# Performance work log

Measured on AMD Instinct MI355X. Metric: run time of the kernel, lower is better.

## Reference

```python
import jax, jax.numpy as jnp
import numpy as np

L, Q, B, F = 4096, 16, 4096, 2048


def setup_inputs() -> dict:
    key = jax.random.key(0)
    k1, k2, k3, k4, k5 = jax.random.split(key, 5)
    return {
        "input_features": jax.random.normal(k1, (B, F), dtype=jnp.float32),
        "queues": jax.random.normal(k2, (L, Q, F), dtype=jnp.float32),
        "labels": jax.random.randint(k3, (B,), 0, L, dtype=jnp.int32),
        "current_flags": jax.random.randint(k4, (L,), 0, Q, dtype=jnp.int32),
        "sample_idx": jax.random.randint(k5, (L,), 0, Q, dtype=jnp.int32),
    }


def reference(input_features, queues, labels, current_flags, sample_idx):
    # Faithful to Queues.update(): the momentum blend + normalize on each slot is
    # overwritten by the final `queue[label][flag] = input_feature`, so the net
    # effect is: for each sample i (in order), write input_features[i] into
    # queue[labels[i]] at slot (flags[labels[i]] + rank_i) % Q, where rank_i is
    b, f = input_features.shape
    l, q, _ = queues.shape
    idx = jnp.arange(b, dtype=jnp.int32)

    # rank of each sample within its label group (stable sort trick, no [B,L] one-hot)
    order = jnp.argsort(labels)                                   # stable in jax
    labels_sorted = labels[order]
    start = jax.ops.segment_min(idx, labels_sorted, num_segments=l)
    rank_sorted = idx - start[labels_sorted]
    rank = jnp.zeros((b,), jnp.int32).at[order].set(rank_sorted)

    pos = (current_flags[labels] + rank) % q                      # circular slot per sample

    flat_key = labels * q + pos
    winner = jax.ops.segment_max(idx, flat_key, num_segments=l * q)
    is_winner = winner[flat_key] == idx
    lab_w = jnp.where(is_winner, labels, l)                       # out-of-range -> dropped

    new_queues = queues.at[lab_w, pos].set(input_features, mode="drop")

    # advance circular pointers by per-label counts (state update, as in update())
    counts = jax.ops.segment_sum(jnp.ones((b,), jnp.int32), labels, num_segments=l)
    new_flags = (current_flags + counts) % q  # noqa: F841 (state; not sampled below)

    # get_features(): one random slot per label queue
    out = new_queues[jnp.arange(l), sample_idx]                   # [L, F]
    return out
```

## Files before the change

kernel.cpp:

```cpp
#include <hip/hip_runtime.h>

#define L_ 4096
#define Q_ 16
#define B_ 4096
#define F_ 2048
#define NC 16
#define CS 256


__global__ void k_rank(const int* __restrict__ labels,
                       int* __restrict__ chunkHist,
                       int* __restrict__ localrank,
                       int* __restrict__ winner) {
    __shared__ int lab[CS];
    __shared__ int hist[L_];
    const int c = blockIdx.x;
    const int t = threadIdx.x;
    const int i = c * CS + t;

    winner[i] = -1;

    const int myl = labels[i];
    lab[t] = myl;
    #pragma unroll
    for (int k = 0; k < L_ / CS; ++k) hist[k * CS + t] = 0;
    __syncthreads();

    int r = 0;
    #pragma unroll 8
    for (int j = 0; j < CS; ++j) {
        r += (j < t && lab[j] == myl) ? 1 : 0;
    }
    localrank[i] = r;
    atomicAdd(&hist[myl], 1);
    __syncthreads();

    #pragma unroll
    for (int k = 0; k < L_ / CS; ++k)
        chunkHist[c * L_ + k * CS + t] = hist[k * CS + t];
}

__global__ void k_winner(const int* __restrict__ labels,
                         const int* __restrict__ flags,
                         const int* __restrict__ sidx,
                         const int* __restrict__ chunkHist,
                         const int* __restrict__ localrank,
                         int* __restrict__ winner) {
    const int i = blockIdx.x * blockDim.x + threadIdx.x;
    if (i >= B_) return;
    const int lab = labels[i];
    const int ci = i >> 8;
    int prefix = 0, total = 0;
    #pragma unroll
    for (int c = 0; c < NC; ++c) {
        const int v = chunkHist[c * L_ + lab];
        total += v;
        prefix += (c < ci) ? v : 0;
    }
    const int rank = localrank[i] + prefix;
    const int s = sidx[lab];
    const int fl = flags[lab];
    const int r0 = (s - fl) & (Q_ - 1);
    if (r0 < total) {
        const int rstar = r0 + Q_ * ((total - 1 - r0) >> 4);
        if (rank == rstar) winner[lab] = i;
    }
}

__global__ void k_out(const float* __restrict__ input,
                      const float* __restrict__ queues,
                      const int* __restrict__ sidx,
                      const int* __restrict__ winner,
                      float* __restrict__ out) {
    const int l = blockIdx.x;
    const int w = winner[l];
    const float4* __restrict__ src =
        (w >= 0) ? (const float4*)(input + (size_t)w * F_)
                 : (const float4*)(queues + ((size_t)l * Q_ + sidx[l]) * F_);
    float4* __restrict__ dst = (float4*)(out + (size_t)l * F_);
    const int t = threadIdx.x;
    dst[t]       = src[t];
    dst[t + 256] = src[t + 256];
}

extern "C" void kernel_launch(void* const* d_in, const int* in_sizes, int n_in,
                              void* d_out, int out_size, void* d_ws, size_t ws_size,
                              hipStream_t stream) {
    const float* input  = (const float*)d_in[0];
    const float* queues = (const float*)d_in[1];
    const int*   labels = (const int*)d_in[2];
    const int*   flags  = (const int*)d_in[3];
    const int*   sidx   = (const int*)d_in[4];
    float* out = (float*)d_out;

    int* chunkHist = (int*)d_ws;
    int* winner    = chunkHist + NC * L_;
    int* localrank = winner + L_;

    k_rank<<<NC, CS, 0, stream>>>(labels, chunkHist, localrank, winner);
    k_winner<<<(B_ + 255) / 256, 256, 0, stream>>>(labels, flags, sidx, chunkHist, localrank, winner);
    k_out<<<L_, 256, 0, stream>>>(input, queues, sidx, winner, out);
}
```

Baseline: 612.0 us.

## Fuse rank, winner and gather kernels into one per-label block kernel

Replaces the three-kernel pipeline (chunk histogram, winner resolution, gather) with a single kernel. Each of the L blocks scans all B labels, counts matches for its own label with a bitmask plus a wave prefix scan, and finds the winning sample directly before copying the row. This removes two launches, the workspace round trips and the serial 16-block histogram stage. In exchange, every block rereads the full 16 KB labels array, which gives redundant L×B comparisons that should be served from cache.

Result: faster. 598.1 us (-2.3%).

```diff
diff --git a/kernel.cpp b/kernel.cpp
--- a/kernel.cpp
+++ b/kernel.cpp
@@ -4,81 +4,73 @@
 #define Q_ 16
 #define B_ 4096
 #define F_ 2048
-#define NC 16
-#define CS 256
 
+__global__ __launch_bounds__(256) void k_fused(
+    const float* __restrict__ input,
+    const float* __restrict__ queues,
+    const int*   __restrict__ labels,
+    const int*   __restrict__ flags,
+    const int*   __restrict__ sidx,
+    float*       __restrict__ out)
+{
+    const int l    = blockIdx.x;
+    const int t    = threadIdx.x;
+    const int lane = t & 63;
+    const int wave = t >> 6;
 
-__global__ void k_rank(const int* __restrict__ labels,
-                       int* __restrict__ chunkHist,
-                       int* __restrict__ localrank,
-                       int* __restrict__ winner) {
-    __shared__ int lab[CS];
-    __shared__ int hist[L_];
-    const int c = blockIdx.x;
-    const int t = threadIdx.x;
-    const int i = c * CS + t;
+    const int4* lp = (const int4*)(labels + t * 16);
+    int4 a = lp[0], b = lp[1], c = lp[2], d = lp[3];
+    unsigned mask = 0;
+    mask |= (unsigned)(a.x == l) << 0;  mask |= (unsigned)(a.y == l) << 1;
+    mask |= (unsigned)(a.z == l) << 2;  mask |= (unsigned)(a.w == l) << 3;
+    mask |= (unsigned)(b.x == l) << 4;  mask |= (unsigned)(b.y == l) << 5;
+    mask |= (unsigned)(b.z == l) << 6;  mask |= (unsigned)(b.w == l) << 7;
+    mask |= (unsigned)(c.x == l) << 8;  mask |= (unsigned)(c.y == l) << 9;
+    mask |= (unsigned)(c.z == l) << 10; mask |= (unsigned)(c.w == l) << 11;
+    mask |= (unsigned)(d.x == l) << 12; mask |= (unsigned)(d.y == l) << 13;
+    mask |= (unsigned)(d.z == l) << 14; mask |= (unsigned)(d.w == l) << 15;
+    const int m = __popc(mask);
 
-    winner[i] = -1;
+    int incl = m;
+    #pragma unroll
+    for (int off = 1; off < 64; off <<= 1) {
+        int v = __shfl_up(incl, off, 64);
+        incl += (lane >= off) ? v : 0;
+    }
 
-    const int myl = labels[i];
-    lab[t] = myl;
-    #pragma unroll
-    for (int k = 0; k < L_ / CS; ++k) hist[k * CS + t] = 0;
+    __shared__ int wtot[4];
+    __shared__ int s_win;
+    if (lane == 63) wtot[wave] = incl;
+    if (t == 0) s_win = -1;
     __syncthreads();
 
-    int r = 0;
-    #pragma unroll 8
-    for (int j = 0; j < CS; ++j) {
-        r += (j < t && lab[j] == myl) ? 1 : 0;
+    int woff = 0, total = 0;
+    #pragma unroll
+    for (int w2 = 0; w2 < 4; ++w2) {
+        const int v = wtot[w2];
+        total += v;
+        woff += (w2 < wave) ? v : 0;
     }
-    localrank[i] = r;
-    atomicAdd(&hist[myl], 1);
+    const int p = woff + incl - m;
+
+    const int s  = sidx[l];
+    const int r0 = (s - flags[l]) & (Q_ - 1);
+    if (r0 < total) {
+        const int rstar = r0 + (((total - 1 - r0) >> 4) << 4);
+        if (rstar >= p && rstar < p + m) {
+            int need = rstar - p;
+            unsigned mm = mask;
+            while (need--) mm &= mm - 1;
+            s_win = t * 16 + (__ffs(mm) - 1);
+        }
+    }
     __syncthreads();
 
-    #pragma unroll
-    for (int k = 0; k < L_ / CS; ++k)
-        chunkHist[c * L_ + k * CS + t] = hist[k * CS + t];
-}
-
-__global__ void k_winner(const int* __restrict__ labels,
-                         const int* __restrict__ flags,
-                         const int* __restrict__ sidx,
-                         const int* __restrict__ chunkHist,
-                         const int* __restrict__ localrank,
-                         int* __restrict__ winner) {
-    const int i = blockIdx.x * blockDim.x + threadIdx.x;
-    if (i >= B_) return;
-    const int lab = labels[i];
-    const int ci = i >> 8;
-    int prefix = 0, total = 0;
-    #pragma unroll
-    for (int c = 0; c < NC; ++c) {
-        const int v = chunkHist[c * L_ + lab];
-        total += v;
-        prefix += (c < ci) ? v : 0;
-    }
-    const int rank = localrank[i] + prefix;
-    const int s = sidx[lab];
-    const int fl = flags[lab];
-    const int r0 = (s - fl) & (Q_ - 1);
-    if (r0 < total) {
-        const int rstar = r0 + Q_ * ((total - 1 - r0) >> 4);
-        if (rank == rstar) winner[lab] = i;
-    }
-}
-
-__global__ void k_out(const float* __restrict__ input,
-                      const float* __restrict__ queues,
-                      const int* __restrict__ sidx,
-                      const int* __restrict__ winner,
-                      float* __restrict__ out) {
-    const int l = blockIdx.x;
-    const int w = winner[l];
+    const int w = s_win;
     const float4* __restrict__ src =
         (w >= 0) ? (const float4*)(input + (size_t)w * F_)
-                 : (const float4*)(queues + ((size_t)l * Q_ + sidx[l]) * F_);
+                 : (const float4*)(queues + ((size_t)l * Q_ + s) * F_);
     float4* __restrict__ dst = (float4*)(out + (size_t)l * F_);
-    const int t = threadIdx.x;
     dst[t]       = src[t];
     dst[t + 256] = src[t + 256];
 }
@@ -93,11 +85,5 @@
     const int*   sidx   = (const int*)d_in[4];
     float* out = (float*)d_out;
 
-    int* chunkHist = (int*)d_ws;
-    int* winner    = chunkHist + NC * L_;
-    int* localrank = winner + L_;
-
-    k_rank<<<NC, CS, 0, stream>>>(labels, chunkHist, localrank, winner);
-    k_winner<<<(B_ + 255) / 256, 256, 0, stream>>>(labels, flags, sidx, chunkHist, localrank, winner);
-    k_out<<<L_, 256, 0, stream>>>(input, queues, sidx, winner, out);
+    k_fused<<<L_, 256, 0, stream>>>(input, queues, labels, flags, sidx, out);
 }
```
